# Optimization experiments

Hardware: AMD Instinct MI355X
Metric: run time of the kernel (lower is better)

Reference implementation:

```python
import jax, jax.numpy as jnp
import numpy as np


def _generate_fitpack_knots(x, k):
    # FITPACK-style knots: k+1 copies of x[0], k+1 copies of x[-1],
    # interior knots are length-k moving averages of x[1:-1].
    n = x.shape[0]
    n_interior = n - k - 1  # number of interior knots
    win_sum = x[1:1 + n_interior]
    for j in range(1, k):  # k is a small static int (e.g. 3)
        win_sum = win_sum + x[1 + j:1 + j + n_interior]
    interior = win_sum / k
    head = jnp.full((k + 1,), x[0], dtype=x.dtype)
    tail = jnp.full((k + 1,), x[-1], dtype=x.dtype)
    return jnp.concatenate([head, interior, tail])


def _safe_div(num, den):
    # torch.nan_to_num_(num/den): 0/0 -> 0, x/0 -> 0
    den_safe = jnp.where(den == 0, jnp.ones_like(den), den)
    return jnp.where(den == 0, jnp.zeros_like(num), num / den_safe)


def _bspline_basis_natural(x, k, t):
    n = x.shape[0]
    m = t.shape[0] - k - 1
    xc = x[:, None]  # [n, 1]
    # zeroth-order basis: indicator of knot interval, with boundary fixes
    b = ((t[None, :m] <= xc) & (xc < t[None, 1:m + 1])).astype(x.dtype)
    b = b.at[:, 0].set(jnp.where(x < t[1], jnp.ones_like(x), b[:, 0]))
    b = b.at[:, -1].set(jnp.where(x >= t[-2], jnp.ones_like(x), b[:, -1]))
    zeros_col = jnp.zeros((n, 1), dtype=x.dtype)
    # de Boor recursion over degree d = 1..k (k is static and small)
    for d in range(1, k + 1):
        L = _safe_div(xc - t[None, :m], (t[d:m + d] - t[:m])[None, :])
        R = _safe_div(t[None, d + 1:m + d + 1] - xc,
                      (t[d + 1:m + d + 1] - t[1:m + 1])[None, :])
        b_shift = jnp.concatenate([b[:, 1:], zeros_col], axis=1)
        b = L * b + R * b_shift
    return b  # [n, m]


def setup_inputs() -> dict:
    key = jax.random.key(0)
    N = 4096
    x = jnp.sort(jax.random.uniform(key, (N,), dtype=jnp.float32) * 10.0)
    s = jnp.asarray(1e-3, dtype=jnp.float32)
    return {"x": x, "s": s, "k": 3}


def reference(x, s, k):
    knots = _generate_fitpack_knots(x, k)
    basis_matrix = _bspline_basis_natural(x, k, knots)  # [n, m]
    m = basis_matrix.shape[-1]
    B_T_B = basis_matrix.T @ basis_matrix + s * jnp.eye(m, dtype=basis_matrix.dtype)
    return (knots, basis_matrix, B_T_B)
```

## Files before the change

kernel.cpp:

```cpp
#include <hip/hip_runtime.h>

#define K 3

__device__ __forceinline__ float tfun(const float* __restrict__ x, int j, int N) {
    if (j <= K) return x[0];
    if (j >= N) return x[N - 1];
    return (x[j - 3] + x[j - 2] + x[j - 1]) / 3.0f;
}

__device__ __forceinline__ int j0_of(const float* __restrict__ x, int i, int N) {
    float xi = x[i];
    int j0 = i + 1;
    if (tfun(x, i + 2, N) <= xi) j0 = i + 2;
    if (tfun(x, i + 3, N) <= xi) j0 = i + 3;
    if (j0 > N - 1) j0 = N - 1;
    if (j0 < K) j0 = K;
    return j0;
}

__device__ __forceinline__ float4 deboor(const float* __restrict__ x, float xi,
                                         int j0, int N) {
    int c0 = j0 - K;
    float b[K + 2];
    #pragma unroll
    for (int w = 0; w < K + 2; ++w) b[w] = 0.f;
    b[K] = 1.f;
    #pragma unroll
    for (int d = 1; d <= K; ++d) {
        float nb[K + 1];
        #pragma unroll
        for (int w = 0; w <= K; ++w) {
            int j = c0 + w;
            float tj   = tfun(x, j, N);
            float tjd  = tfun(x, j + d, N);
            float tj1  = tfun(x, j + 1, N);
            float tjd1 = tfun(x, j + d + 1, N);
            float denL = tjd - tj;
            float L = (denL == 0.f) ? 0.f : (xi - tj) / denL;
            float denR = tjd1 - tj1;
            float R = (denR == 0.f) ? 0.f : (tjd1 - xi) / denR;
            nb[w] = L * b[w] + R * b[w + 1];
        }
        #pragma unroll
        for (int w = 0; w <= K; ++w) b[w] = nb[w];
    }
    return make_float4(b[0], b[1], b[2], b[3]);
}

#define B1 64
#define HALO 4

__global__ __launch_bounds__(B1) void k1_precompute(const float* __restrict__ x,
                                                    const float* __restrict__ s_ptr,
                                                    float* __restrict__ out_knots,
                                                    float* __restrict__ vals,
                                                    int* __restrict__ j0arr,
                                                    float* __restrict__ band, int N) {
    __shared__ float4 lv[73];
    __shared__ int lj[73];
    int t = threadIdx.x;
    int bs = blockIdx.x * B1;

    for (int k = t; k < 73; k += B1) {
        int rb = bs - HALO + k;
        if (rb >= 0 && rb < N) {
            int j0 = j0_of(x, rb, N);
            lj[k] = j0;
            lv[k] = deboor(x, x[rb], j0, N);
        } else {
            lj[k] = -1000000;
            lv[k] = make_float4(0.f, 0.f, 0.f, 0.f);
        }
    }
    __syncthreads();

    int i = bs + t;
    if (i >= N) return;

    out_knots[i] = tfun(x, i, N);
    if (i < K + 1) out_knots[N + i] = x[N - 1];

    int kk = t + HALO;
    int j0i = lj[kk];
    float4 v4i = lv[kk];
    j0arr[i] = j0i;
    *(float4*)(vals + 4 * i) = v4i;

    float acc[2 * K + 1];
    #pragma unroll
    for (int a = 0; a < 2 * K + 1; ++a) acc[a] = 0.f;

    #pragma unroll
    for (int d = -3; d <= 5; ++d) {
        int k2 = kk + d;
        int j0r = lj[k2];
        if (j0r < i || j0r > i + K) continue;
        float4 w4 = lv[k2];
        int wi = i - (j0r - K);
        float v = (wi == 0) ? w4.x : (wi == 1) ? w4.y : (wi == 2) ? w4.z : w4.w;
        #pragma unroll
        for (int o = -K; o <= K; ++o) {
            int wj = wi + o;
            float w = (wj == 0) ? w4.x : (wj == 1) ? w4.y : (wj == 2) ? w4.z
                    : (wj == 3) ? w4.w : 0.f;
            acc[o + K] += v * w;
        }
    }
    acc[K] += *s_ptr;

    *(float4*)(band + i * 8)     = make_float4(acc[0], acc[1], acc[2], acc[3]);
    *(float4*)(band + i * 8 + 4) = make_float4(acc[4], acc[5], acc[6], 0.f);
}

__global__ __launch_bounds__(256) void k2_write(const float* __restrict__ vals,
                                                const int* __restrict__ j0arr,
                                                const float* __restrict__ band,
                                                float* __restrict__ outB,
                                                float* __restrict__ outBTB, int N) {
    int bid = blockIdx.x;
    int tid = threadIdx.x;
    int fpr = N >> 2;

    if (bid < N) {
        int i = bid;
        int c0 = j0arr[i] - K;
        float4 v4 = *(const float4*)(vals + i * 4);
        float4* rowp = (float4*)(outB + (long long)i * N);
        int fw0 = c0 >> 2, fw1 = (c0 + K) >> 2;
        for (int f = tid; f < fpr; f += 256) {
            float4 z = make_float4(0.f, 0.f, 0.f, 0.f);
            if (f == fw0 || f == fw1) {
                int e0 = f * 4;
                float e[4];
                #pragma unroll
                for (int l = 0; l < 4; ++l) {
                    int d = e0 + l - c0;
                    e[l] = (d == 0) ? v4.x : (d == 1) ? v4.y : (d == 2) ? v4.z
                         : (d == 3) ? v4.w : 0.f;
                }
                z = make_float4(e[0], e[1], e[2], e[3]);
            }
            rowp[f] = z;
        }
    } else {
        int ci = bid - N;
        float4 b0 = *(const float4*)(band + ci * 8);
        float4 b1 = *(const float4*)(band + ci * 8 + 4);
        float4* rowp = (float4*)(outBTB + (long long)ci * N);
        int wlo = ci - K; if (wlo < 0) wlo = 0;
        int whi = ci + K; if (whi > N - 1) whi = N - 1;
        int fw0 = wlo >> 2, fw1 = whi >> 2;
        for (int f = tid; f < fpr; f += 256) {
            float4 z = make_float4(0.f, 0.f, 0.f, 0.f);
            if (f >= fw0 && f <= fw1) {
                int e0 = f * 4;
                float e[4];
                #pragma unroll
                for (int l = 0; l < 4; ++l) {
                    int d = e0 + l - ci;
                    e[l] = (d == -3) ? b0.x : (d == -2) ? b0.y : (d == -1) ? b0.z
                         : (d ==  0) ? b0.w : (d ==  1) ? b1.x : (d ==  2) ? b1.y
                         : (d ==  3) ? b1.z : 0.f;
                }
                z = make_float4(e[0], e[1], e[2], e[3]);
            }
            rowp[f] = z;
        }
    }
}

extern "C" void kernel_launch(void* const* d_in, const int* in_sizes, int n_in,
                              void* d_out, int out_size, void* d_ws, size_t ws_size,
                              hipStream_t stream) {
    const float* x = (const float*)d_in[0];
    const float* s = (const float*)d_in[1];
    int N = in_sizes[0];
    int nk = N + K + 1;

    float* out = (float*)d_out;
    float* out_knots = out;
    float* out_B = out + nk;
    float* out_BTB = out_B + (long long)N * N;

    float* band_ws = (float*)d_ws;
    float* vals_ws = band_ws + (long long)N * 8;
    int* j0_ws = (int*)(vals_ws + (long long)N * 4);

    k1_precompute<<<(N + B1 - 1) / B1, B1, 0, stream>>>(x, s, out_knots,
                                                        vals_ws, j0_ws, band_ws, N);
    k2_write<<<2 * N, 256, 0, stream>>>(vals_ws, j0_ws, band_ws, out_B, out_BTB, N);
}
```

Before: 45.79 us.

## Replace dense row-writing kernel with memset plus sparse patch of nonzeros

Drops the second kernel that wrote every element of the two N×N output matrices (mostly zeros) with per-element select logic. The whole output is now zero-filled with hipMemsetAsync, and the precompute kernel writes only the four B values and seven banded BTB values per row directly. This removes the workspace round trip and the branchy zero-writing pass. In exchange it relies on the runtime memset's bandwidth, adds a second ordered pass over a small set of scattered uncoalesced stores, and zeroes the knots region redundantly.

```diff
diff --git a/kernel.cpp b/kernel.cpp
--- a/kernel.cpp
+++ b/kernel.cpp
@@ -50,12 +50,11 @@
 #define B1 64
 #define HALO 4
 
-__global__ __launch_bounds__(B1) void k1_precompute(const float* __restrict__ x,
+__global__ __launch_bounds__(B1) void patch_windows(const float* __restrict__ x,
                                                     const float* __restrict__ s_ptr,
                                                     float* __restrict__ out_knots,
-                                                    float* __restrict__ vals,
-                                                    int* __restrict__ j0arr,
-                                                    float* __restrict__ band, int N) {
+                                                    float* __restrict__ outB,
+                                                    float* __restrict__ outBTB, int N) {
     __shared__ float4 lv[73];
     __shared__ int lj[73];
     int t = threadIdx.x;
@@ -83,8 +82,9 @@
     int kk = t + HALO;
     int j0i = lj[kk];
     float4 v4i = lv[kk];
-    j0arr[i] = j0i;
-    *(float4*)(vals + 4 * i) = v4i;
+
+    float* bp = outB + (long long)i * N + (j0i - K);
+    bp[0] = v4i.x; bp[1] = v4i.y; bp[2] = v4i.z; bp[3] = v4i.w;
 
     float acc[2 * K + 1];
     #pragma unroll
@@ -108,64 +108,11 @@
     }
     acc[K] += *s_ptr;
 
-    *(float4*)(band + i * 8)     = make_float4(acc[0], acc[1], acc[2], acc[3]);
-    *(float4*)(band + i * 8 + 4) = make_float4(acc[4], acc[5], acc[6], 0.f);
-}
-
-__global__ __launch_bounds__(256) void k2_write(const float* __restrict__ vals,
-                                                const int* __restrict__ j0arr,
-                                                const float* __restrict__ band,
-                                                float* __restrict__ outB,
-                                                float* __restrict__ outBTB, int N) {
-    int bid = blockIdx.x;
-    int tid = threadIdx.x;
-    int fpr = N >> 2;
-
-    if (bid < N) {
-        int i = bid;
-        int c0 = j0arr[i] - K;
-        float4 v4 = *(const float4*)(vals + i * 4);
-        float4* rowp = (float4*)(outB + (long long)i * N);
-        int fw0 = c0 >> 2, fw1 = (c0 + K) >> 2;
-        for (int f = tid; f < fpr; f += 256) {
-            float4 z = make_float4(0.f, 0.f, 0.f, 0.f);
-            if (f == fw0 || f == fw1) {
-                int e0 = f * 4;
-                float e[4];
-                #pragma unroll
-                for (int l = 0; l < 4; ++l) {
-                    int d = e0 + l - c0;
-                    e[l] = (d == 0) ? v4.x : (d == 1) ? v4.y : (d == 2) ? v4.z
-                         : (d == 3) ? v4.w : 0.f;
-                }
-                z = make_float4(e[0], e[1], e[2], e[3]);
-            }
-            rowp[f] = z;
-        }
-    } else {
-        int ci = bid - N;
-        float4 b0 = *(const float4*)(band + ci * 8);
-        float4 b1 = *(const float4*)(band + ci * 8 + 4);
-        float4* rowp = (float4*)(outBTB + (long long)ci * N);
-        int wlo = ci - K; if (wlo < 0) wlo = 0;
-        int whi = ci + K; if (whi > N - 1) whi = N - 1;
-        int fw0 = wlo >> 2, fw1 = whi >> 2;
-        for (int f = tid; f < fpr; f += 256) {
-            float4 z = make_float4(0.f, 0.f, 0.f, 0.f);
-            if (f >= fw0 && f <= fw1) {
-                int e0 = f * 4;
-                float e[4];
-                #pragma unroll
-                for (int l = 0; l < 4; ++l) {
-                    int d = e0 + l - ci;
-                    e[l] = (d == -3) ? b0.x : (d == -2) ? b0.y : (d == -1) ? b0.z
-                         : (d ==  0) ? b0.w : (d ==  1) ? b1.x : (d ==  2) ? b1.y
-                         : (d ==  3) ? b1.z : 0.f;
-                }
-                z = make_float4(e[0], e[1], e[2], e[3]);
-            }
-            rowp[f] = z;
-        }
+    long long base = (long long)i * N;
+    #pragma unroll
+    for (int d = -K; d <= K; ++d) {
+        int c = i + d;
+        if (c >= 0 && c < N) outBTB[base + c] = acc[d + K];
     }
 }
 
@@ -182,11 +129,8 @@
     float* out_B = out + nk;
     float* out_BTB = out_B + (long long)N * N;
 
-    float* band_ws = (float*)d_ws;
-    float* vals_ws = band_ws + (long long)N * 8;
-    int* j0_ws = (int*)(vals_ws + (long long)N * 4);
+    hipMemsetAsync(d_out, 0, (size_t)out_size * sizeof(float), stream);
 
-    k1_precompute<<<(N + B1 - 1) / B1, B1, 0, stream>>>(x, s, out_knots,
-                                                        vals_ws, j0_ws, band_ws, N);
-    k2_write<<<2 * N, 256, 0, stream>>>(vals_ws, j0_ws, band_ws, out_B, out_BTB, N);
+    patch_windows<<<(N + B1 - 1) / B1, B1, 0, stream>>>(x, s, out_knots,
+                                                        out_B, out_BTB, N);
 }
```

New measurement: 45.08 us. About the same (-1.6%).
